# Kernel optimization log

Hardware: AMD Instinct MI355X
Metric: run time of the kernel (lower is better)

Reference implementation:

```python
import jax, jax.numpy as jnp
import numpy as np

BIT_WIDTH = 8
UP = float(2 ** (BIT_WIDTH - 1) - 1)   # 127
LOW = float(-(2 ** (BIT_WIDTH - 1)))   # -128


def setup_inputs() -> dict:
    key = jax.random.key(0)
    k1, k2, k3, k4, k5 = jax.random.split(key, 5)
    B, Cin, H, W = 32, 256, 56, 56
    Cout, kH, kW = 256, 3, 3
    x = jax.random.normal(k1, (B, Cin, H, W), dtype=jnp.float32)
    weight = jax.random.normal(k2, (Cout, Cin, kH, kW), dtype=jnp.float32) * 0.05
    bias = jax.random.normal(k3, (Cout,), dtype=jnp.float32) * 0.1
    # positive quantization scales (roughly map |w|~0.15, |x|~3 into int8 range)
    sw = jax.random.uniform(k4, (Cout,), minval=200.0, maxval=800.0, dtype=jnp.float32)
    sx = jax.random.uniform(k5, (1,), minval=20.0, maxval=40.0, dtype=jnp.float32)
    return {"x": x, "weight": weight, "bias": bias, "sw": sw, "sx": sx}


def reference(x, weight, bias, sw, sx):
    """QConv2d forward in q_inference (quant-simulation) mode:
    per-out-channel fake-quantize weight, per-tensor fake-quantize input,
    then float conv2d + bias. jnp.round matches torch.round (half-to-even)."""
    swb = sw[:, None, None, None]                      # [Cout,1,1,1]
    q_w = jnp.round(jnp.clip(weight * swb, LOW, UP)) / swb
    q_x = jnp.round(jnp.clip(x * sx[0], LOW, UP)) / sx[0]
    out = jax.lax.conv_general_dilated(
        q_x, q_w,
        window_strides=(1, 1),
        padding=((1, 1), (1, 1)),
        dimension_numbers=("NCHW", "OIHW", "NCHW"),
    )
    return out + bias[None, :, None, None]
```

## Files before the change

kernel.cpp:

```cpp
#include <hip/hip_runtime.h>
#include <stdint.h>

typedef int int32x4 __attribute__((ext_vector_type(4)));

#define HW_        3136
#define CHW_       802816
#define HP_        58
#define WP_        58
#define PLANE_PIX  107648ull
#define PLANE_B    (PLANE_PIX*16)
#define QXP_BYTES  (16ull*PLANE_B)
#define QWT_BYTES  (9ull*16*256*16)

__device__ __forceinline__ signed char quant8(float v, float s) {
    float t = v * s;
    t = fmaxf(t, -128.0f);
    t = fminf(t, 127.0f);
    return (signed char)(int)rintf(t);
}

__global__ __launch_bounds__(256) void halo_rows_kernel(signed char* __restrict__ qxp2) {
    int idx = blockIdx.x*256 + threadIdx.x;
    if (idx < 16*32*2*58) {
        int cq = idx / (32*2*58);
        int r  = idx % (32*2*58);
        int b  = r / (2*58);
        int t  = r % (2*58);
        int hp = (t / 58) * (HP_-1);
        int wp = t % 58;
        *(int32x4*)(qxp2 + ((size_t)cq*PLANE_PIX + (size_t)(b*HP_+hp)*WP_ + wp)*16)
            = (int32x4){0,0,0,0};
    }
}

__global__ __launch_bounds__(256) void quant_w_kernel(
    const float* __restrict__ wgt, const float* __restrict__ sw,
    signed char* __restrict__ qwT2)
{
    __shared__ __align__(16) signed char lw[9*272];
    const int o = blockIdx.x, c = threadIdx.x;
    const float s = sw[o];
    const float* wp = wgt + ((size_t)o*256 + c)*9;
    #pragma unroll
    for (int kk = 0; kk < 9; ++kk)
        lw[kk*272 + c] = quant8(wp[kk], s);
    __syncthreads();
    if (c < 144) {
        int kk = c / 16, cq = c - kk*16;
        int32x4 v = *(const int32x4*)&lw[kk*272 + cq*16];
        *(int32x4*)(qwT2 + ((size_t)(kk*16 + cq)*256 + o)*16) = v;
    }
}

__global__ __launch_bounds__(256) void quant_x_kernel(
    const float* __restrict__ x, const float* __restrict__ sx,
    signed char* __restrict__ qxp2)
{
    const int tid = threadIdx.x;
    const int bh = blockIdx.x;
    const int b = bh / 56, h = bh % 56;
    const float s = sx[0];
    if (tid < 224) {
        const int w  = tid % 56;
        const int cg = tid / 56;
        const size_t xrow = (size_t)b*CHW_ + (size_t)h*56 + w;
        const size_t pb = ((size_t)(b*HP_ + h + 1)*WP_ + 1 + w)*16;
        #pragma unroll
        for (int k = 0; k < 4; ++k) {
            const int cq = cg*4 + k;
            const float* xp = x + xrow + (size_t)(cq*16)*HW_;
            int pk[4];
            #pragma unroll
            for (int g = 0; g < 4; ++g) {
                int b0 = (unsigned char)quant8(xp[(size_t)(4*g+0)*HW_], s);
                int b1 = (unsigned char)quant8(xp[(size_t)(4*g+1)*HW_], s);
                int b2 = (unsigned char)quant8(xp[(size_t)(4*g+2)*HW_], s);
                int b3 = (unsigned char)quant8(xp[(size_t)(4*g+3)*HW_], s);
                pk[g] = b0 | (b1 << 8) | (b2 << 16) | (b3 << 24);
            }
            *(int32x4*)(qxp2 + (size_t)cq*PLANE_B + pb) = (int32x4){pk[0],pk[1],pk[2],pk[3]};
        }
    } else {
        int t2 = tid - 224;
        int cq = t2 >> 1, wp = (t2 & 1) * (WP_-1);
        const size_t rowpix = (size_t)(b*HP_ + h + 1)*WP_;
        *(int32x4*)(qxp2 + ((size_t)cq*PLANE_PIX + rowpix + wp)*16) = (int32x4){0,0,0,0};
    }
}

__device__ __forceinline__ void load16_lds(const void* g, void* l) {
    __builtin_amdgcn_global_load_lds(
        (const unsigned int*)g,
        reinterpret_cast<__attribute__((address_space(3))) unsigned int*>(
            reinterpret_cast<uintptr_t>(l)),
        16, 0, 0);
}

__global__ __launch_bounds__(256, 4) void conv_kernel(
    const signed char* __restrict__ qxp2, const signed char* __restrict__ qwT2,
    const float* __restrict__ sw, const float* __restrict__ bias,
    const float* __restrict__ sx, float* __restrict__ out)
{
    __shared__ __align__(16) signed char smem[33792];
    __shared__ float invS[128];
    __shared__ float biasS[128];
    signed char* ldsA = smem;
    signed char* ldsB = smem + 16384;

    const int tid  = threadIdx.x;
    const int wave = tid >> 6;
    const int lane = tid & 63;
    const int quad = lane >> 4;
    const int l15  = lane & 15;
    const int s0 = blockIdx.x * 128;
    const int o0 = blockIdx.y * 128;

    if (tid < 128) {
        float s = sw[o0 + tid];
        invS[tid]  = 1.0f / (s * sx[0]);
        biasS[tid] = bias[o0 + tid];
    }

    const unsigned sp0 = (unsigned)(s0 + lane);
    const unsigned sp1 = (unsigned)(s0 + 64 + lane);
    unsigned b0 = sp0 / HW_, r0 = sp0 - b0*HW_;
    unsigned b1 = sp1 / HW_, r1 = sp1 - b1*HW_;
    unsigned h0 = r0 / 56,   w0 = r0 - h0*56;
    unsigned h1 = r1 / 56,   w1 = r1 - h1*56;
    const size_t bOff0 = ((size_t)(b0*HP_ + h0)*WP_ + w0)*16;
    const size_t bOff1 = ((size_t)(b1*HP_ + h1)*WP_ + w1)*16;
    const size_t aOff0 = (size_t)(o0 + lane)*16;
    const size_t aOff1 = aOff0 + 1024;

    int32x4 acc[4][4];
    #pragma unroll
    for (int i = 0; i < 4; ++i)
        #pragma unroll
        for (int j = 0; j < 4; ++j)
            acc[i][j] = (int32x4){0,0,0,0};

    const int wo = (wave & 1) << 6;
    const int wn = (wave >> 1) << 6;

    for (int kk = 0; kk < 9; ++kk) {
        const size_t kshift = (size_t)((kk/3)*WP_ + (kk%3))*16;
        const size_t aKK = (size_t)kk*16*4096;
        #pragma unroll
        for (int hf = 0; hf < 2; ++hf) {
            const int cq0 = hf*8;
            #pragma unroll
            for (int t = 0; t < 2; ++t) {
                const int kc = 2*wave + t;
                const int cq = cq0 + kc;
                const signed char* aG = qwT2 + aKK + (size_t)cq*4096;
                load16_lds(aG + aOff0, ldsA + kc*2048);
                load16_lds(aG + aOff1, ldsA + kc*2048 + 1024);
                const signed char* bG = qxp2 + (size_t)cq*PLANE_B + kshift;
                load16_lds(bG + bOff0, ldsB + kc*2048);
                load16_lds(bG + bOff1, ldsB + kc*2048 + 1024);
            }
            __syncthreads();
            #pragma unroll
            for (int ks = 0; ks < 2; ++ks) {
                const int ck = (ks*4 + quad)*2048;
                int32x4 af[4], bf[4];
                #pragma unroll
                for (int t = 0; t < 4; ++t) {
                    af[t] = *(const int32x4*)&ldsA[ck + (wo + t*16 + l15)*16];
                    bf[t] = *(const int32x4*)&ldsB[ck + (wn + t*16 + l15)*16];
                }
                #pragma unroll
                for (int mt = 0; mt < 4; ++mt)
                    #pragma unroll
                    for (int nt = 0; nt < 4; ++nt)
                        acc[mt][nt] = __builtin_amdgcn_mfma_i32_16x16x64_i8(
                            af[mt], bf[nt], acc[mt][nt], 0, 0, 0);
            }
            __syncthreads();
        }
    }

    float* lt = (float*)smem;
    #pragma unroll
    for (int p = 0; p < 2; ++p) {
        __syncthreads();
        if ((wave & 1) == p) {
            #pragma unroll
            for (int mt = 0; mt < 4; ++mt)
                #pragma unroll
                for (int nt = 0; nt < 4; ++nt)
                    #pragma unroll
                    for (int r = 0; r < 4; ++r)
                        lt[(mt*16 + quad*4 + r)*132 + wn + nt*16 + l15]
                            = (float)acc[mt][nt][r];
        }
        __syncthreads();
        #pragma unroll
        for (int i = 0; i < 8; ++i) {
            int idx = i*256 + tid;
            int o = idx >> 5;
            int c = idx & 31;
            float4 v = *(const float4*)&lt[o*132 + 4*c];
            int ol = p*64 + o;
            float is = invS[ol], bs = biasS[ol];
            unsigned sp = (unsigned)(s0 + 4*c);
            unsigned b  = sp / HW_;
            unsigned pos = sp - b*HW_;
            float4 wv;
            wv.x = fmaf(v.x, is, bs); wv.y = fmaf(v.y, is, bs);
            wv.z = fmaf(v.z, is, bs); wv.w = fmaf(v.w, is, bs);
            *(float4*)(out + (size_t)b*CHW_ + (size_t)(o0 + ol)*HW_ + pos) = wv;
        }
    }
}

extern "C" void kernel_launch(void* const* d_in, const int* in_sizes, int n_in,
                              void* d_out, int out_size, void* d_ws, size_t ws_size,
                              hipStream_t stream)
{
    (void)in_sizes; (void)n_in; (void)out_size; (void)ws_size;
    const float* x    = (const float*)d_in[0];
    const float* wgt  = (const float*)d_in[1];
    const float* bias = (const float*)d_in[2];
    const float* sw   = (const float*)d_in[3];
    const float* sx   = (const float*)d_in[4];
    float* out = (float*)d_out;

    signed char* qxp2 = (signed char*)d_ws;
    signed char* qwT2 = qxp2 + QXP_BYTES;

    halo_rows_kernel<<<232, 256, 0, stream>>>(qxp2);
    quant_w_kernel<<<256, 256, 0, stream>>>(wgt, sw, qwT2);
    quant_x_kernel<<<1792, 256, 0, stream>>>(x, sx, qxp2);
    conv_kernel<<<dim3(784, 2), 256, 0, stream>>>(qxp2, qwT2, sw, bias, sx, out);
}
```

Before: 283.9 us.

## Double-buffer conv LDS stages with prefetch and swizzle block order

The conv kernel's K loop becomes 18 stages over two 32KB LDS buffers. Each stage issues the async global-to-LDS loads for the next stage before running MFMAs on the current one, using a partial vmcnt wait plus raw barriers, and raises wave priority around the MFMA block. A 1D grid with an XCD-aware swizzle maps blocks to spatial/output tiles. This aims to hide load latency and improve cache locality, but doubling LDS to 64KB lowers occupancy from 4 to 2 blocks per CU.

```diff
diff --git a/kernel.cpp b/kernel.cpp
--- a/kernel.cpp
+++ b/kernel.cpp
@@ -96,30 +96,23 @@
         16, 0, 0);
 }
 
-__global__ __launch_bounds__(256, 4) void conv_kernel(
+__global__ __launch_bounds__(256, 2) void conv_kernel(
     const signed char* __restrict__ qxp2, const signed char* __restrict__ qwT2,
     const float* __restrict__ sw, const float* __restrict__ bias,
     const float* __restrict__ sx, float* __restrict__ out)
 {
-    __shared__ __align__(16) signed char smem[33792];
-    __shared__ float invS[128];
-    __shared__ float biasS[128];
-    signed char* ldsA = smem;
-    signed char* ldsB = smem + 16384;
+    __shared__ __align__(16) signed char smem[65536];
 
     const int tid  = threadIdx.x;
     const int wave = tid >> 6;
     const int lane = tid & 63;
     const int quad = lane >> 4;
     const int l15  = lane & 15;
-    const int s0 = blockIdx.x * 128;
-    const int o0 = blockIdx.y * 128;
-
-    if (tid < 128) {
-        float s = sw[o0 + tid];
-        invS[tid]  = 1.0f / (s * sx[0]);
-        biasS[tid] = bias[o0 + tid];
-    }
+
+    const int bid = blockIdx.x;
+    const int swz = (bid & 7) * 196 + (bid >> 3);
+    const int s0  = (swz >> 1) * 128;
+    const int o0  = (swz & 1) * 128;
 
     const unsigned sp0 = (unsigned)(s0 + lane);
     const unsigned sp1 = (unsigned)(s0 + 64 + lane);
@@ -142,45 +135,69 @@
     const int wo = (wave & 1) << 6;
     const int wn = (wave >> 1) << 6;
 
-    for (int kk = 0; kk < 9; ++kk) {
+    auto stage = [&](int st, signed char* bufA, signed char* bufB) {
+        const int kk  = st >> 1;
+        const int cq0 = (st & 1) * 8;
         const size_t kshift = (size_t)((kk/3)*WP_ + (kk%3))*16;
         const size_t aKK = (size_t)kk*16*4096;
         #pragma unroll
-        for (int hf = 0; hf < 2; ++hf) {
-            const int cq0 = hf*8;
-            #pragma unroll
-            for (int t = 0; t < 2; ++t) {
-                const int kc = 2*wave + t;
-                const int cq = cq0 + kc;
-                const signed char* aG = qwT2 + aKK + (size_t)cq*4096;
-                load16_lds(aG + aOff0, ldsA + kc*2048);
-                load16_lds(aG + aOff1, ldsA + kc*2048 + 1024);
-                const signed char* bG = qxp2 + (size_t)cq*PLANE_B + kshift;
-                load16_lds(bG + bOff0, ldsB + kc*2048);
-                load16_lds(bG + bOff1, ldsB + kc*2048 + 1024);
+        for (int t = 0; t < 2; ++t) {
+            const int kc = 2*wave + t;
+            const int cq = cq0 + kc;
+            const signed char* aG = qwT2 + aKK + (size_t)cq*4096;
+            load16_lds(aG + aOff0, bufA + kc*2048);
+            load16_lds(aG + aOff1, bufA + kc*2048 + 1024);
+            const signed char* bG = qxp2 + (size_t)cq*PLANE_B + kshift;
+            load16_lds(bG + bOff0, bufB + kc*2048);
+            load16_lds(bG + bOff1, bufB + kc*2048 + 1024);
+        }
+    };
+
+    stage(0, smem, smem + 16384);
+
+    for (int st = 0; st < 18; ++st) {
+        signed char* ldsA = smem + ((st & 1) << 15);
+        signed char* ldsB = ldsA + 16384;
+        if (st < 17) {
+            signed char* nb = smem + (((st + 1) & 1) << 15);
+            stage(st + 1, nb, nb + 16384);
+            asm volatile("s_waitcnt vmcnt(8)");
+        } else {
+            asm volatile("s_waitcnt vmcnt(0)");
+        }
+        __builtin_amdgcn_s_barrier();
+        __builtin_amdgcn_sched_barrier(0);
+        #pragma unroll
+        for (int ks = 0; ks < 2; ++ks) {
+            const int ck = (ks*4 + quad)*2048;
+            int32x4 af[4], bf[4];
+            #pragma unroll
+            for (int t = 0; t < 4; ++t) {
+                af[t] = *(const int32x4*)&ldsA[ck + (wo + t*16 + l15)*16];
+                bf[t] = *(const int32x4*)&ldsB[ck + (wn + t*16 + l15)*16];
             }
-            __syncthreads();
-            #pragma unroll
-            for (int ks = 0; ks < 2; ++ks) {
-                const int ck = (ks*4 + quad)*2048;
-                int32x4 af[4], bf[4];
+            __builtin_amdgcn_s_setprio(1);
+            #pragma unroll
+            for (int mt = 0; mt < 4; ++mt)
                 #pragma unroll
-                for (int t = 0; t < 4; ++t) {
-                    af[t] = *(const int32x4*)&ldsA[ck + (wo + t*16 + l15)*16];
-                    bf[t] = *(const int32x4*)&ldsB[ck + (wn + t*16 + l15)*16];
-                }
-                #pragma unroll
-                for (int mt = 0; mt < 4; ++mt)
-                    #pragma unroll
-                    for (int nt = 0; nt < 4; ++nt)
-                        acc[mt][nt] = __builtin_amdgcn_mfma_i32_16x16x64_i8(
-                            af[mt], bf[nt], acc[mt][nt], 0, 0, 0);
-            }
-            __syncthreads();
-        }
-    }
-
-    float* lt = (float*)smem;
+                for (int nt = 0; nt < 4; ++nt)
+                    acc[mt][nt] = __builtin_amdgcn_mfma_i32_16x16x64_i8(
+                        af[mt], bf[nt], acc[mt][nt], 0, 0, 0);
+            __builtin_amdgcn_s_setprio(0);
+        }
+        __builtin_amdgcn_sched_barrier(0);
+        __builtin_amdgcn_s_barrier();
+    }
+    asm volatile("" ::: "memory");
+
+    float* lt    = (float*)smem;
+    float* invS  = (float*)(smem + 33792);
+    float* biasS = (float*)(smem + 34304);
+    if (tid < 128) {
+        float s = sw[o0 + tid];
+        invS[tid]  = 1.0f / (s * sx[0]);
+        biasS[tid] = bias[o0 + tid];
+    }
     #pragma unroll
     for (int p = 0; p < 2; ++p) {
         __syncthreads();
@@ -232,5 +249,5 @@
     halo_rows_kernel<<<232, 256, 0, stream>>>(qxp2);
     quant_w_kernel<<<256, 256, 0, stream>>>(wgt, sw, qwT2);
     quant_x_kernel<<<1792, 256, 0, stream>>>(x, sx, qxp2);
-    conv_kernel<<<dim3(784, 2), 256, 0, stream>>>(qxp2, qwT2, sw, bias, sx, out);
-}
+    conv_kernel<<<1568, 256, 0, stream>>>(qxp2, qwT2, sw, bias, sx, out);
+}
```

Measured after the change: 271.2 us. 4.5% less time.
